# Performance work log

Hardware: AMD Instinct MI355X
Metric: run time of the kernel (lower is better)

## Reference

```python
import jax, jax.numpy as jnp
import numpy as np

B, S, N, D = 4, 30, 2000, 32
HD = 64        # hidden_dim
HEADS = 4
E = 128000


def setup_inputs() -> dict:
    key = jax.random.key(0)
    ks = iter(jax.random.split(key, 48))
    p = lambda shape: jax.random.normal(next(ks), shape, dtype=jnp.float32) * 0.05
    inp = {}
    inp["x_seq"] = jax.random.normal(next(ks), (B, S, N, D), dtype=jnp.float32)
    inp["edge_index"] = jax.random.randint(next(ks), (2, E), 0, N)
    # Bidirectional 2-layer LSTM params (torch gate order i,f,g,o; b = b_ih+b_hh)
    for l, din in [(0, D), (1, 2 * HD)]:
        for d in ("f", "b"):
            inp[f"W_ih_{l}{d}"] = p((4 * HD, din))
            inp[f"W_hh_{l}{d}"] = p((4 * HD, HD))
            inp[f"bias_{l}{d}"] = p((4 * HD,))
    # GAT layer 0: in 2*HD, layer 1: in HD; heads=4, head dim HD, head-averaged output
    inp["gW0"] = p((2 * HD, HEADS * HD))
    inp["ga_src0"] = p((HEADS, HD)); inp["ga_dst0"] = p((HEADS, HD)); inp["gb0"] = p((HD,))
    inp["gW1"] = p((HD, HEADS * HD))
    inp["ga_src1"] = p((HEADS, HD)); inp["ga_dst1"] = p((HEADS, HD)); inp["gb1"] = p((HD,))
    # fc_out: Linear(HD, HD//2) -> ReLU -> Linear(HD//2, 1)
    inp["fW1"] = p((HD // 2, HD)); inp["fb1"] = p((HD // 2,))
    inp["fW2"] = p((1, HD // 2)); inp["fb2"] = p((1,))
    return inp


def _lstm_dir(x, W_ih, W_hh, b, reverse):
    # x: [BN, S, Din] -> hidden states [BN, S, H]
    pre = jnp.einsum('bsd,gd->sbg', x, W_ih) + b  # input projection, [S, BN, 4H]
    BN = x.shape[0]
    H = W_hh.shape[1]

    def step(carry, xt):
        h, c = carry
        g = xt + h @ W_hh.T
        i, f, gg, o = jnp.split(g, 4, axis=-1)
        c = jax.nn.sigmoid(f) * c + jax.nn.sigmoid(i) * jnp.tanh(gg)
        h = jax.nn.sigmoid(o) * jnp.tanh(c)
        return (h, c), h

    init = (jnp.zeros((BN, H), x.dtype), jnp.zeros((BN, H), x.dtype))
    _, hs = jax.lax.scan(step, init, pre, reverse=reverse)
    return jnp.transpose(hs, (1, 0, 2))  # [BN, S, H]


def _gat(x, W, a_src, a_dst, bias, src, dst, num_nodes):
    # edge-wise gather -> attention -> scatter-softmax -> scatter-sum; head-averaged
    Hh, C = a_src.shape
    xp = (x @ W).reshape(-1, Hh, C)                       # [Nn, H, C]
    e = jax.nn.leaky_relu(
        jnp.einsum('nhc,hc->nh', xp, a_src)[src]
        + jnp.einsum('nhc,hc->nh', xp, a_dst)[dst], 0.2)  # [E, H]
    emax = jax.ops.segment_max(e, dst, num_segments=num_nodes)
    w = jnp.exp(e - emax[dst])
    denom = jax.ops.segment_sum(w, dst, num_segments=num_nodes)
    out = jax.ops.segment_sum(w[:, :, None] * xp[src], dst, num_segments=num_nodes)
    out = out / (denom[:, :, None] + 1e-16)
    return out.mean(axis=1) + bias                        # [Nn, C]


def reference(x_seq, edge_index,
              W_ih_0f, W_hh_0f, bias_0f, W_ih_0b, W_hh_0b, bias_0b,
              W_ih_1f, W_hh_1f, bias_1f, W_ih_1b, W_hh_1b, bias_1b,
              gW0, ga_src0, ga_dst0, gb0, gW1, ga_src1, ga_dst1, gb1,
              fW1, fb1, fW2, fb2):
    B_, S_, N_, D_ = x_seq.shape
    x = jnp.transpose(x_seq, (0, 2, 1, 3)).reshape(B_ * N_, S_, D_)
    # bidirectional 2-layer LSTM (eval mode, dropout off)
    h0 = jnp.concatenate([_lstm_dir(x, W_ih_0f, W_hh_0f, bias_0f, False),
                          _lstm_dir(x, W_ih_0b, W_hh_0b, bias_0b, True)], axis=-1)
    h1 = jnp.concatenate([_lstm_dir(h0, W_ih_1f, W_hh_1f, bias_1f, False),
                          _lstm_dir(h0, W_ih_1b, W_hh_1b, bias_1b, True)], axis=-1)
    last = h1[:, -1, :]                                   # [B*N, 2*HD]
    # batch edge_index with per-graph node offsets + self loops (PyG default)
    offs = (jnp.arange(B_) * N_)[None, :, None]
    ei = (edge_index[:, None, :] + offs).reshape(2, -1)
    loops = jnp.arange(B_ * N_)
    src = jnp.concatenate([ei[0], loops])
    dst = jnp.concatenate([ei[1], loops])
    x = jax.nn.relu(_gat(last, gW0, ga_src0, ga_dst0, gb0, src, dst, B_ * N_))
    x = jax.nn.relu(_gat(x, gW1, ga_src1, ga_dst1, gb1, src, dst, B_ * N_))
    x = x.reshape(B_, N_, -1).mean(axis=1)                # mean-pool over nodes
    h = jax.nn.relu(x @ fW1.T + fb1)
    return h @ fW2.T + fb2                                # [B, 1]
```

## Files before the change

kernel.cpp:

```cpp
#include <hip/hip_runtime.h>
#include <cstdint>

#define NN 2000
#define BB 4
#define SEQ 30
#define NODES (BB*NN)
#define EPB 128000
#define NEDGE (BB*EPB + NODES)

constexpr size_t WP0 = 96 * 256;
constexpr size_t WP1 = 192 * 256;
constexpr size_t OFF_WP0F = 0;
constexpr size_t OFF_WP0B = OFF_WP0F + WP0;
constexpr size_t OFF_WP1F = OFF_WP0B + WP0;
constexpr size_t OFF_WP1B = OFF_WP1F + WP1;
constexpr size_t OFF_BP0F = OFF_WP1B + WP1;
constexpr size_t OFF_BP0B = OFF_BP0F + 256;
constexpr size_t OFF_BP1F = OFF_BP0B + 256;
constexpr size_t OFF_BP1B = OFF_BP1F + 256;
constexpr size_t OFF_H0   = OFF_BP1B + 256;
constexpr size_t OFF_LAST = OFF_H0 + (size_t)NODES * SEQ * 128;
constexpr size_t OFF_XP   = OFF_LAST + (size_t)NODES * 128;
constexpr size_t OFF_AS   = OFF_XP + (size_t)NODES * 256;
constexpr size_t OFF_AD   = OFF_AS + (size_t)NODES * 4;
constexpr size_t OFF_F1   = OFF_AD + (size_t)NODES * 4;
constexpr size_t OFF_F2   = OFF_F1 + (size_t)NODES * 64;
constexpr size_t OFF_INT  = OFF_F2 + (size_t)NODES * 64;
constexpr size_t IOFF_CNT  = 0;
constexpr size_t IOFF_OFFS = 8192;
constexpr size_t IOFF_CUR  = 16384;
constexpr size_t IOFF_SSRC = 24576;

__device__ __forceinline__ float rdlane(float v, int k) {
  return __uint_as_float((unsigned)__builtin_amdgcn_readlane((int)__float_as_uint(v), k));
}
__device__ __forceinline__ float sigf(float x) { return 1.f / (1.f + __expf(-x)); }
__device__ __forceinline__ float tanhfast(float x) { return 1.f - 2.f / (__expf(2.f * x) + 1.f); }
__device__ __forceinline__ void fma4(float4& a, float s, const float4& w) {
  a.x = fmaf(s, w.x, a.x); a.y = fmaf(s, w.y, a.y);
  a.z = fmaf(s, w.z, a.z); a.w = fmaf(s, w.w, a.w);
}

__global__ void permute_w(const float* __restrict__ Wih, const float* __restrict__ Whh,
                          const float* __restrict__ bias, float* __restrict__ wp,
                          float* __restrict__ bp, int DIN) {
  const int k = blockIdx.x;
  const int c = threadIdx.x;
  const int jj = c >> 2, q = c & 3;
  const int g = q * 64 + jj;
  const float v = (k < DIN) ? Wih[g * DIN + k] : Whh[g * 64 + (k - DIN)];
  wp[k * 256 + c] = v;
  if (k == 0) bp[c] = bias[g];
}

template<int DIN, bool WRITE_ALL>
__global__ __launch_bounds__(256)
void lstm_scan(const float* __restrict__ xin,
               const float* __restrict__ wpF, const float* __restrict__ wpB,
               const float* __restrict__ bpF, const float* __restrict__ bpB,
               float* __restrict__ hout) {
  constexpr int M = 8;
  __shared__ float whh[64 * 256];
  const int dir = blockIdx.y;
  const float* __restrict__ wp = dir ? wpB : wpF;
  const float* __restrict__ bp = dir ? bpB : bpF;
  {
    const float4* src = (const float4*)(wp + DIN * 256);
    float4* dst = (float4*)whh;
    for (int idx = threadIdx.x; idx < 64 * 256 / 4; idx += 256) dst[idx] = src[idx];
  }
  __syncthreads();

  const int wv = threadIdx.x >> 6;
  const int j  = threadIdx.x & 63;
  const int n0 = (blockIdx.x * 4 + wv) * M;
  const int dirOff = dir * 64;
  const float4 bias4 = *(const float4*)(bp + 4 * j);

  float hreg[M], creg[M];
#pragma unroll
  for (int m = 0; m < M; ++m) { hreg[m] = 0.f; creg[m] = 0.f; }

  int xbase[M];
#pragma unroll
  for (int m = 0; m < M; ++m) {
    const int n = n0 + m;
    if (DIN == 32) {
      const int b = n / NN, node = n - b * NN;
      xbase[m] = (b * SEQ * NN + node) * 32 + (j & 31);
    } else {
      xbase[m] = n * SEQ * 128 + j;
    }
  }

  int steps = SEQ;
  const bool rev = (dir != 0);
  if (!WRITE_ALL && dir) steps = 1;

  for (int t = 0; t < steps; ++t) {
    const int s = rev ? (SEQ - 1 - t) : t;

    float xr0[M], xr1[M];
#pragma unroll
    for (int m = 0; m < M; ++m) {
      if (DIN == 32) {
        xr0[m] = xin[xbase[m] + s * (NN * 32)];
        xr1[m] = 0.f;
      } else {
        xr0[m] = xin[xbase[m] + s * 128];
        xr1[m] = xin[xbase[m] + s * 128 + 64];
      }
    }

    float4 acc[M];
#pragma unroll
    for (int m = 0; m < M; ++m) acc[m] = bias4;

    if (DIN == 32) {
#pragma unroll 8
      for (int k = 0; k < 32; ++k) {
        const float4 w4 = *(const float4*)(wp + k * 256 + 4 * j);
#pragma unroll
        for (int m = 0; m < M; ++m) fma4(acc[m], rdlane(xr0[m], k), w4);
      }
    } else {
#pragma unroll 8
      for (int k = 0; k < 64; ++k) {
        const float4 w4 = *(const float4*)(wp + k * 256 + 4 * j);
#pragma unroll
        for (int m = 0; m < M; ++m) fma4(acc[m], rdlane(xr0[m], k), w4);
      }
#pragma unroll 8
      for (int k = 0; k < 64; ++k) {
        const float4 w4 = *(const float4*)(wp + (64 + k) * 256 + 4 * j);
#pragma unroll
        for (int m = 0; m < M; ++m) fma4(acc[m], rdlane(xr1[m], k), w4);
      }
    }

#pragma unroll 8
    for (int k = 0; k < 64; ++k) {
      const float4 w4 = *(const float4*)(whh + k * 256 + 4 * j);
#pragma unroll
      for (int m = 0; m < M; ++m) fma4(acc[m], rdlane(hreg[m], k), w4);
    }

#pragma unroll
    for (int m = 0; m < M; ++m) {
      const float iv = sigf(acc[m].x);
      const float fv = sigf(acc[m].y);
      const float gv = tanhfast(acc[m].z);
      const float ov = sigf(acc[m].w);
      const float c = fv * creg[m] + iv * gv;
      const float h = ov * tanhfast(c);
      creg[m] = c; hreg[m] = h;
      if (WRITE_ALL) hout[((size_t)(n0 + m) * SEQ + s) * 128 + dirOff + j] = h;
    }
  }
  if (!WRITE_ALL) {
#pragma unroll
    for (int m = 0; m < M; ++m) hout[(size_t)(n0 + m) * 128 + dirOff + j] = hreg[m];
  }
}

__global__ void csr_zero(int* cnt) {
  const int i = blockIdx.x * 256 + threadIdx.x;
  if (i < NODES + 1) cnt[i] = 0;
}
__global__ void csr_count(const int* __restrict__ ei, int* __restrict__ cnt) {
  const int e = blockIdx.x * 256 + threadIdx.x;
  if (e >= NEDGE) return;
  int dst;
  if (e < BB * EPB) { const int b = e / EPB, i = e - b * EPB; dst = ei[EPB + i] + b * NN; }
  else dst = e - BB * EPB;
  atomicAdd(&cnt[dst], 1);
}
__global__ void csr_scan(const int* __restrict__ cnt, int* __restrict__ offs, int* __restrict__ cur) {
  __shared__ int sums[1024];
  const int t = threadIdx.x;
  const int base = t * 8;
  int loc[8]; int s = 0;
#pragma unroll
  for (int i = 0; i < 8; ++i) {
    const int v = (base + i < NODES) ? cnt[base + i] : 0;
    loc[i] = s; s += v;
  }
  sums[t] = s; __syncthreads();
  for (int off = 1; off < 1024; off <<= 1) {
    int v = 0;
    if (t >= off) v = sums[t - off];
    __syncthreads();
    sums[t] += v;
    __syncthreads();
  }
  const int pre = (t == 0) ? 0 : sums[t - 1];
#pragma unroll
  for (int i = 0; i < 8; ++i) {
    if (base + i < NODES) { const int o = pre + loc[i]; offs[base + i] = o; cur[base + i] = o; }
  }
  if (t == 1023) offs[NODES] = sums[1023];
}
__global__ void csr_fill(const int* __restrict__ ei, int* __restrict__ cur, int* __restrict__ ssrc) {
  const int e = blockIdx.x * 256 + threadIdx.x;
  if (e >= NEDGE) return;
  int src, dst;
  if (e < BB * EPB) {
    const int b = e / EPB, i = e - b * EPB;
    src = ei[i] + b * NN; dst = ei[EPB + i] + b * NN;
  } else { src = dst = e - BB * EPB; }
  const int pos = atomicAdd(&cur[dst], 1);
  ssrc[pos] = src;
}

template<int F>
__global__ __launch_bounds__(256)
void gat_prep(const float* __restrict__ feat, const float* __restrict__ gW,
              const float* __restrict__ asrc, const float* __restrict__ adst,
              float* __restrict__ xp, float* __restrict__ as_, float* __restrict__ ad_) {
  __shared__ float xrow[8 * F];
  const int n0 = blockIdx.x * 8;
  for (int idx = threadIdx.x; idx < 8 * F; idx += 256) xrow[idx] = feat[(size_t)n0 * F + idx];
  __syncthreads();
  const int g = threadIdx.x;
  float acc[8];
#pragma unroll
  for (int m = 0; m < 8; ++m) acc[m] = 0.f;
  for (int d = 0; d < F; ++d) {
    const float w = gW[d * 256 + g];
#pragma unroll
    for (int m = 0; m < 8; ++m) acc[m] = fmaf(xrow[m * F + d], w, acc[m]);
  }
#pragma unroll
  for (int m = 0; m < 8; ++m) xp[(size_t)(n0 + m) * 256 + g] = acc[m];
  const float av = asrc[g], dv = adst[g];
  const int h = g >> 6;
#pragma unroll
  for (int m = 0; m < 8; ++m) {
    float s1 = acc[m] * av, s2 = acc[m] * dv;
#pragma unroll
    for (int off = 1; off < 64; off <<= 1) {
      s1 += __shfl_xor(s1, off);
      s2 += __shfl_xor(s2, off);
    }
    if ((g & 63) == 0) {
      as_[(n0 + m) * 4 + h] = s1;
      ad_[(n0 + m) * 4 + h] = s2;
    }
  }
}

__global__ __launch_bounds__(256)
void gat_agg(const int* __restrict__ offs, const int* __restrict__ ssrc,
             const float* __restrict__ as_, const float* __restrict__ ad_,
             const float* __restrict__ xp, const float* __restrict__ gbias,
             float* __restrict__ outf) {
  const int v = blockIdx.x * 4 + (threadIdx.x >> 6);
  const int lane = threadIdx.x & 63;
  const int beg = offs[v], end = offs[v + 1];
  const float4 adv = *(const float4*)(ad_ + v * 4);

  float m0 = -1e30f, m1 = -1e30f, m2 = -1e30f, m3 = -1e30f;
  for (int i = beg + lane; i < end; i += 64) {
    const int sn = ssrc[i];
    const float4 asv = *(const float4*)(as_ + sn * 4);
    float e;
    e = asv.x + adv.x; e = e > 0.f ? e : 0.2f * e; m0 = fmaxf(m0, e);
    e = asv.y + adv.y; e = e > 0.f ? e : 0.2f * e; m1 = fmaxf(m1, e);
    e = asv.z + adv.z; e = e > 0.f ? e : 0.2f * e; m2 = fmaxf(m2, e);
    e = asv.w + adv.w; e = e > 0.f ? e : 0.2f * e; m3 = fmaxf(m3, e);
  }
#pragma unroll
  for (int off = 1; off < 64; off <<= 1) {
    m0 = fmaxf(m0, __shfl_xor(m0, off));
    m1 = fmaxf(m1, __shfl_xor(m1, off));
    m2 = fmaxf(m2, __shfl_xor(m2, off));
    m3 = fmaxf(m3, __shfl_xor(m3, off));
  }

  float a0 = 0, a1 = 0, a2 = 0, a3 = 0, d0 = 0, d1 = 0, d2 = 0, d3 = 0;
  for (int i = beg; i < end; ++i) {
    const int sn = ssrc[i];
    const float4 asv = *(const float4*)(as_ + sn * 4);
    const float* xr = xp + (size_t)sn * 256;
    float e, w;
    e = asv.x + adv.x; e = e > 0.f ? e : 0.2f * e; w = __expf(e - m0); d0 += w; a0 = fmaf(w, xr[lane], a0);
    e = asv.y + adv.y; e = e > 0.f ? e : 0.2f * e; w = __expf(e - m1); d1 += w; a1 = fmaf(w, xr[64 + lane], a1);
    e = asv.z + adv.z; e = e > 0.f ? e : 0.2f * e; w = __expf(e - m2); d2 += w; a2 = fmaf(w, xr[128 + lane], a2);
    e = asv.w + adv.w; e = e > 0.f ? e : 0.2f * e; w = __expf(e - m3); d3 += w; a3 = fmaf(w, xr[192 + lane], a3);
  }
  const float r = 0.25f * (a0 / (d0 + 1e-16f) + a1 / (d1 + 1e-16f) +
                           a2 / (d2 + 1e-16f) + a3 / (d3 + 1e-16f)) + gbias[lane];
  outf[(size_t)v * 64 + lane] = fmaxf(r, 0.f);
}

__global__ void final_mlp(const float* __restrict__ feat2,
                          const float* __restrict__ fW1, const float* __restrict__ fb1,
                          const float* __restrict__ fW2, const float* __restrict__ fb2,
                          float* __restrict__ out) {
  const int b = blockIdx.x;
  __shared__ float part[4][64];
  __shared__ float y[64];
  __shared__ float hh[32];
  const int t = threadIdx.x;
  const int c = t & 63, r = t >> 6;
  float s = 0.f;
  for (int i = r; i < NN; i += 4) s += feat2[(size_t)(b * NN + i) * 64 + c];
  part[r][c] = s; __syncthreads();
  if (t < 64) y[t] = (part[0][t] + part[1][t] + part[2][t] + part[3][t]) * (1.0f / NN);
  __syncthreads();
  if (t < 32) {
    float a = fb1[t];
    for (int cc = 0; cc < 64; ++cc) a = fmaf(y[cc], fW1[t * 64 + cc], a);
    hh[t] = fmaxf(a, 0.f);
  }
  __syncthreads();
  if (t == 0) {
    float o = fb2[0];
    for (int jj = 0; jj < 32; ++jj) o = fmaf(hh[jj], fW2[jj], o);
    out[b] = o;
  }
}

extern "C" void kernel_launch(void* const* d_in, const int* in_sizes, int n_in,
                              void* d_out, int out_size, void* d_ws, size_t ws_size,
                              hipStream_t stream) {
  const float* x_seq = (const float*)d_in[0];
  const int*   ei    = (const int*)d_in[1];
  const float* Wih0f = (const float*)d_in[2];  const float* Whh0f = (const float*)d_in[3];  const float* b0f = (const float*)d_in[4];
  const float* Wih0b = (const float*)d_in[5];  const float* Whh0b = (const float*)d_in[6];  const float* b0b = (const float*)d_in[7];
  const float* Wih1f = (const float*)d_in[8];  const float* Whh1f = (const float*)d_in[9];  const float* b1f = (const float*)d_in[10];
  const float* Wih1b = (const float*)d_in[11]; const float* Whh1b = (const float*)d_in[12]; const float* b1b = (const float*)d_in[13];
  const float* gW0 = (const float*)d_in[14]; const float* gas0 = (const float*)d_in[15];
  const float* gad0 = (const float*)d_in[16]; const float* gb0 = (const float*)d_in[17];
  const float* gW1 = (const float*)d_in[18]; const float* gas1 = (const float*)d_in[19];
  const float* gad1 = (const float*)d_in[20]; const float* gb1 = (const float*)d_in[21];
  const float* fW1 = (const float*)d_in[22]; const float* fb1 = (const float*)d_in[23];
  const float* fW2 = (const float*)d_in[24]; const float* fb2 = (const float*)d_in[25];

  float* ws = (float*)d_ws;
  float* wp0f = ws + OFF_WP0F; float* wp0b = ws + OFF_WP0B;
  float* wp1f = ws + OFF_WP1F; float* wp1b = ws + OFF_WP1B;
  float* bp0f = ws + OFF_BP0F; float* bp0b = ws + OFF_BP0B;
  float* bp1f = ws + OFF_BP1F; float* bp1b = ws + OFF_BP1B;
  float* h0   = ws + OFF_H0;   float* last = ws + OFF_LAST;
  float* xp   = ws + OFF_XP;   float* as_  = ws + OFF_AS;  float* ad_ = ws + OFF_AD;
  float* f1   = ws + OFF_F1;   float* f2   = ws + OFF_F2;
  int* iws  = (int*)(ws + OFF_INT);
  int* cnt  = iws + IOFF_CNT;  int* offs = iws + IOFF_OFFS;
  int* cur  = iws + IOFF_CUR;  int* ssrc = iws + IOFF_SSRC;

  permute_w<<<96, 256, 0, stream>>>(Wih0f, Whh0f, b0f, wp0f, bp0f, 32);
  permute_w<<<96, 256, 0, stream>>>(Wih0b, Whh0b, b0b, wp0b, bp0b, 32);
  permute_w<<<192, 256, 0, stream>>>(Wih1f, Whh1f, b1f, wp1f, bp1f, 128);
  permute_w<<<192, 256, 0, stream>>>(Wih1b, Whh1b, b1b, wp1b, bp1b, 128);

  lstm_scan<32, true><<<dim3(250, 2), 256, 0, stream>>>(x_seq, wp0f, wp0b, bp0f, bp0b, h0);
  lstm_scan<128, false><<<dim3(250, 2), 256, 0, stream>>>(h0, wp1f, wp1b, bp1f, bp1b, last);

  csr_zero<<<32, 256, 0, stream>>>(cnt);
  csr_count<<<(NEDGE + 255) / 256, 256, 0, stream>>>(ei, cnt);
  csr_scan<<<1, 1024, 0, stream>>>(cnt, offs, cur);
  csr_fill<<<(NEDGE + 255) / 256, 256, 0, stream>>>(ei, cur, ssrc);

  gat_prep<128><<<1000, 256, 0, stream>>>(last, gW0, gas0, gad0, xp, as_, ad_);
  gat_agg<<<2000, 256, 0, stream>>>(offs, ssrc, as_, ad_, xp, gb0, f1);
  gat_prep<64><<<1000, 256, 0, stream>>>(f1, gW1, gas1, gad1, xp, as_, ad_);
  gat_agg<<<2000, 256, 0, stream>>>(offs, ssrc, as_, ad_, xp, gb1, f2);

  final_mlp<<<4, 256, 0, stream>>>(f2, fW1, fb1, fW2, fb2, (float*)d_out);
}
```

Baseline: 1.288 ms.

## Convert LSTM scan to packed fp16 dot2 with LDS-resident weights

Weights, inputs and the hidden state are packed into fp16 pairs, and the LSTM matmuls use v_dot2 (fdot2) with fp32 accumulation, halving the multiply-accumulate count and memory traffic. All input and recurrent weights now sit in LDS, and the next step's input is prefetched. Blocks grow to 512 threads with 4 nodes per wave instead of 8, and the layer-0 hidden sequence is stored as packed fp16. This reduces precision of the LSTM inputs and states, which may affect accuracy.

```diff
diff --git a/kernel.cpp b/kernel.cpp
--- a/kernel.cpp
+++ b/kernel.cpp
@@ -8,141 +8,153 @@
 #define EPB 128000
 #define NEDGE (BB*EPB + NODES)
 
-constexpr size_t WP0 = 96 * 256;
-constexpr size_t WP1 = 192 * 256;
-constexpr size_t OFF_WP0F = 0;
-constexpr size_t OFF_WP0B = OFF_WP0F + WP0;
-constexpr size_t OFF_WP1F = OFF_WP0B + WP0;
-constexpr size_t OFF_WP1B = OFF_WP1F + WP1;
-constexpr size_t OFF_BP0F = OFF_WP1B + WP1;
-constexpr size_t OFF_BP0B = OFF_BP0F + 256;
-constexpr size_t OFF_BP1F = OFF_BP0B + 256;
-constexpr size_t OFF_BP1B = OFF_BP1F + 256;
-constexpr size_t OFF_H0   = OFF_BP1B + 256;
-constexpr size_t OFF_LAST = OFF_H0 + (size_t)NODES * SEQ * 128;
-constexpr size_t OFF_XP   = OFF_LAST + (size_t)NODES * 128;
-constexpr size_t OFF_AS   = OFF_XP + (size_t)NODES * 256;
-constexpr size_t OFF_AD   = OFF_AS + (size_t)NODES * 4;
-constexpr size_t OFF_F1   = OFF_AD + (size_t)NODES * 4;
-constexpr size_t OFF_F2   = OFF_F1 + (size_t)NODES * 64;
-constexpr size_t OFF_INT  = OFF_F2 + (size_t)NODES * 64;
+constexpr size_t U_WPH0F = 0;
+constexpr size_t U_WPH0B = U_WPH0F + 48 * 256;
+constexpr size_t U_WPH1F = U_WPH0B + 48 * 256;
+constexpr size_t U_WPH1B = U_WPH1F + 96 * 256;
+constexpr size_t U_BP0F  = U_WPH1B + 96 * 256;
+constexpr size_t U_BP0B  = U_BP0F + 256;
+constexpr size_t U_BP1F  = U_BP0B + 256;
+constexpr size_t U_BP1B  = U_BP1F + 256;
+constexpr size_t U_XPK   = U_BP1B + 256;
+constexpr size_t U_H0P   = U_XPK + (size_t)NODES * SEQ * 16;
+constexpr size_t U_LAST  = U_H0P + (size_t)NODES * SEQ * 64;
+constexpr size_t U_XP    = U_LAST + (size_t)NODES * 128;
+constexpr size_t U_AS    = U_XP + (size_t)NODES * 256;
+constexpr size_t U_AD    = U_AS + (size_t)NODES * 4;
+constexpr size_t U_F1    = U_AD + (size_t)NODES * 4;
+constexpr size_t U_F2    = U_F1 + (size_t)NODES * 64;
+constexpr size_t U_INT   = U_F2 + (size_t)NODES * 64;
 constexpr size_t IOFF_CNT  = 0;
 constexpr size_t IOFF_OFFS = 8192;
 constexpr size_t IOFF_CUR  = 16384;
 constexpr size_t IOFF_SSRC = 24576;
 
-__device__ __forceinline__ float rdlane(float v, int k) {
-  return __uint_as_float((unsigned)__builtin_amdgcn_readlane((int)__float_as_uint(v), k));
+typedef _Float16 h2_t __attribute__((ext_vector_type(2)));
+
+#if __has_builtin(__builtin_amdgcn_fdot2)
+__device__ __forceinline__ float fdot2u(uint32_t a, uint32_t b, float c) {
+  return __builtin_amdgcn_fdot2(__builtin_bit_cast(h2_t, a), __builtin_bit_cast(h2_t, b), c, false);
+}
+#else
+__device__ __forceinline__ float fdot2u(uint32_t a, uint32_t b, float c) {
+  h2_t x = __builtin_bit_cast(h2_t, a), y = __builtin_bit_cast(h2_t, b);
+  return fmaf((float)x[1], (float)y[1], fmaf((float)x[0], (float)y[0], c));
+}
+#endif
+__device__ __forceinline__ uint32_t pk16(float a, float b) {
+  return __builtin_bit_cast(uint32_t, __builtin_amdgcn_cvt_pkrtz(a, b));
+}
+__device__ __forceinline__ uint32_t rdlu(uint32_t v, int k) {
+  return (uint32_t)__builtin_amdgcn_readlane((int)v, k);
 }
 __device__ __forceinline__ float sigf(float x) { return 1.f / (1.f + __expf(-x)); }
 __device__ __forceinline__ float tanhfast(float x) { return 1.f - 2.f / (__expf(2.f * x) + 1.f); }
-__device__ __forceinline__ void fma4(float4& a, float s, const float4& w) {
-  a.x = fmaf(s, w.x, a.x); a.y = fmaf(s, w.y, a.y);
-  a.z = fmaf(s, w.z, a.z); a.w = fmaf(s, w.w, a.w);
-}
-
-__global__ void permute_w(const float* __restrict__ Wih, const float* __restrict__ Whh,
-                          const float* __restrict__ bias, float* __restrict__ wp,
-                          float* __restrict__ bp, int DIN) {
-  const int k = blockIdx.x;
+
+__global__ void permute_pack(const float* __restrict__ Wih, const float* __restrict__ Whh,
+                             const float* __restrict__ bias, uint32_t* __restrict__ wph,
+                             float* __restrict__ bp, int DIN) {
+  const int kp = blockIdx.x;
   const int c = threadIdx.x;
-  const int jj = c >> 2, q = c & 3;
-  const int g = q * 64 + jj;
-  const float v = (k < DIN) ? Wih[g * DIN + k] : Whh[g * 64 + (k - DIN)];
-  wp[k * 256 + c] = v;
-  if (k == 0) bp[c] = bias[g];
-}
-
-template<int DIN, bool WRITE_ALL>
-__global__ __launch_bounds__(256)
-void lstm_scan(const float* __restrict__ xin,
-               const float* __restrict__ wpF, const float* __restrict__ wpB,
+  const int j = c >> 2, q = c & 3;
+  const int g = q * 64 + j;
+  const int k0 = 2 * kp;
+  float a, b;
+  if (k0 < DIN) { a = Wih[g * DIN + k0]; b = Wih[g * DIN + k0 + 1]; }
+  else { const int r = k0 - DIN; a = Whh[g * 64 + r]; b = Whh[g * 64 + r + 1]; }
+  wph[kp * 256 + c] = pk16(a, b);
+  if (kp == 0) bp[c] = bias[g];
+}
+
+__global__ void pack_x(const float* __restrict__ x, uint32_t* __restrict__ out, int n) {
+  const int i = blockIdx.x * 256 + threadIdx.x;
+  if (i < n) out[i] = pk16(x[2 * i], x[2 * i + 1]);
+}
+
+template<int DIN, bool WRITE_ALL, int M>
+__global__ __launch_bounds__(512)
+void lstm_scan(const uint32_t* __restrict__ xpk,
+               const uint32_t* __restrict__ wpF, const uint32_t* __restrict__ wpB,
                const float* __restrict__ bpF, const float* __restrict__ bpB,
-               float* __restrict__ hout) {
-  constexpr int M = 8;
-  __shared__ float whh[64 * 256];
+               float* __restrict__ lastout, uint32_t* __restrict__ hpkout) {
+  constexpr int KPX = DIN / 2;
+  constexpr int KP  = KPX + 32;
+  __shared__ __align__(16) uint32_t wph[KP * 256];
   const int dir = blockIdx.y;
-  const float* __restrict__ wp = dir ? wpB : wpF;
+  const uint32_t* __restrict__ wp = dir ? wpB : wpF;
   const float* __restrict__ bp = dir ? bpB : bpF;
-  {
-    const float4* src = (const float4*)(wp + DIN * 256);
-    float4* dst = (float4*)whh;
-    for (int idx = threadIdx.x; idx < 64 * 256 / 4; idx += 256) dst[idx] = src[idx];
-  }
+  for (int idx = threadIdx.x; idx < KP * 64; idx += 512)
+    ((uint4*)wph)[idx] = ((const uint4*)wp)[idx];
   __syncthreads();
 
   const int wv = threadIdx.x >> 6;
   const int j  = threadIdx.x & 63;
-  const int n0 = (blockIdx.x * 4 + wv) * M;
-  const int dirOff = dir * 64;
+  const int n0 = (blockIdx.x * 8 + wv) * M;
   const float4 bias4 = *(const float4*)(bp + 4 * j);
 
   float hreg[M], creg[M];
-#pragma unroll
-  for (int m = 0; m < M; ++m) { hreg[m] = 0.f; creg[m] = 0.f; }
-
+  uint32_t hpk[M];
+#pragma unroll
+  for (int m = 0; m < M; ++m) { hreg[m] = 0.f; creg[m] = 0.f; hpk[m] = 0u; }
+
+  constexpr int XS = (DIN == 32) ? NN * 16 : 64;
   int xbase[M];
 #pragma unroll
   for (int m = 0; m < M; ++m) {
     const int n = n0 + m;
     if (DIN == 32) {
       const int b = n / NN, node = n - b * NN;
-      xbase[m] = (b * SEQ * NN + node) * 32 + (j & 31);
+      xbase[m] = (b * SEQ * NN + node) * 16 + (j & 15);
     } else {
-      xbase[m] = n * SEQ * 128 + j;
-    }
-  }
-
-  int steps = SEQ;
+      xbase[m] = (n * SEQ) * 64 + j;
+    }
+  }
+
   const bool rev = (dir != 0);
-  if (!WRITE_ALL && dir) steps = 1;
-
-  for (int t = 0; t < steps; ++t) {
-    const int s = rev ? (SEQ - 1 - t) : t;
-
-    float xr0[M], xr1[M];
-#pragma unroll
-    for (int m = 0; m < M; ++m) {
-      if (DIN == 32) {
-        xr0[m] = xin[xbase[m] + s * (NN * 32)];
-        xr1[m] = 0.f;
-      } else {
-        xr0[m] = xin[xbase[m] + s * 128];
-        xr1[m] = xin[xbase[m] + s * 128 + 64];
+  const int steps = (!WRITE_ALL && rev) ? 1 : SEQ;
+  const int sstep = rev ? -1 : 1;
+  int s = rev ? SEQ - 1 : 0;
+
+  uint32_t xu[M];
+#pragma unroll
+  for (int m = 0; m < M; ++m) xu[m] = xpk[xbase[m] + s * XS];
+
+  for (int t = 0; t < steps; ++t, s += sstep) {
+    uint32_t xun[M];
+#pragma unroll
+    for (int m = 0; m < M; ++m) xun[m] = xu[m];
+    if (t + 1 < steps) {
+#pragma unroll
+      for (int m = 0; m < M; ++m) xun[m] = xpk[xbase[m] + (s + sstep) * XS];
+    }
+
+    float4 acc[M];
+#pragma unroll
+    for (int m = 0; m < M; ++m) acc[m] = bias4;
+
+#pragma unroll 2
+    for (int kp = 0; kp < KPX; ++kp) {
+      const uint4 w4 = *(const uint4*)&wph[kp * 256 + 4 * j];
+#pragma unroll
+      for (int m = 0; m < M; ++m) {
+        const uint32_t b2 = rdlu(xu[m], kp);
+        acc[m].x = fdot2u(w4.x, b2, acc[m].x);
+        acc[m].y = fdot2u(w4.y, b2, acc[m].y);
+        acc[m].z = fdot2u(w4.z, b2, acc[m].z);
+        acc[m].w = fdot2u(w4.w, b2, acc[m].w);
       }
     }
-
-    float4 acc[M];
-#pragma unroll
-    for (int m = 0; m < M; ++m) acc[m] = bias4;
-
-    if (DIN == 32) {
-#pragma unroll 8
-      for (int k = 0; k < 32; ++k) {
-        const float4 w4 = *(const float4*)(wp + k * 256 + 4 * j);
-#pragma unroll
-        for (int m = 0; m < M; ++m) fma4(acc[m], rdlane(xr0[m], k), w4);
+#pragma unroll 2
+    for (int kh = 0; kh < 32; ++kh) {
+      const uint4 w4 = *(const uint4*)&wph[(KPX + kh) * 256 + 4 * j];
+#pragma unroll
+      for (int m = 0; m < M; ++m) {
+        const uint32_t b2 = rdlu(hpk[m], 2 * kh);
+        acc[m].x = fdot2u(w4.x, b2, acc[m].x);
+        acc[m].y = fdot2u(w4.y, b2, acc[m].y);
+        acc[m].z = fdot2u(w4.z, b2, acc[m].z);
+        acc[m].w = fdot2u(w4.w, b2, acc[m].w);
       }
-    } else {
-#pragma unroll 8
-      for (int k = 0; k < 64; ++k) {
-        const float4 w4 = *(const float4*)(wp + k * 256 + 4 * j);
-#pragma unroll
-        for (int m = 0; m < M; ++m) fma4(acc[m], rdlane(xr0[m], k), w4);
-      }
-#pragma unroll 8
-      for (int k = 0; k < 64; ++k) {
-        const float4 w4 = *(const float4*)(wp + (64 + k) * 256 + 4 * j);
-#pragma unroll
-        for (int m = 0; m < M; ++m) fma4(acc[m], rdlane(xr1[m], k), w4);
-      }
-    }
-
-#pragma unroll 8
-    for (int k = 0; k < 64; ++k) {
-      const float4 w4 = *(const float4*)(whh + k * 256 + 4 * j);
-#pragma unroll
-      for (int m = 0; m < M; ++m) fma4(acc[m], rdlane(hreg[m], k), w4);
     }
 
 #pragma unroll
@@ -154,12 +166,18 @@
       const float c = fv * creg[m] + iv * gv;
       const float h = ov * tanhfast(c);
       creg[m] = c; hreg[m] = h;
-      if (WRITE_ALL) hout[((size_t)(n0 + m) * SEQ + s) * 128 + dirOff + j] = h;
-    }
+      const float hn = __shfl_down(h, 1);
+      hpk[m] = pk16(h, hn);
+      if (WRITE_ALL && (j & 1) == 0)
+        hpkout[((size_t)(n0 + m) * SEQ + s) * 64 + dir * 32 + (j >> 1)] = hpk[m];
+    }
+#pragma unroll
+    for (int m = 0; m < M; ++m) xu[m] = xun[m];
   }
   if (!WRITE_ALL) {
 #pragma unroll
-    for (int m = 0; m < M; ++m) hout[(size_t)(n0 + m) * 128 + dirOff + j] = hreg[m];
+    for (int m = 0; m < M; ++m)
+      lastout[(size_t)(n0 + m) * 128 + dir * 64 + j] = hreg[m];
   }
 }
 
@@ -337,25 +355,30 @@
   const float* fW1 = (const float*)d_in[22]; const float* fb1 = (const float*)d_in[23];
   const float* fW2 = (const float*)d_in[24]; const float* fb2 = (const float*)d_in[25];
 
-  float* ws = (float*)d_ws;
-  float* wp0f = ws + OFF_WP0F; float* wp0b = ws + OFF_WP0B;
-  float* wp1f = ws + OFF_WP1F; float* wp1b = ws + OFF_WP1B;
-  float* bp0f = ws + OFF_BP0F; float* bp0b = ws + OFF_BP0B;
-  float* bp1f = ws + OFF_BP1F; float* bp1b = ws + OFF_BP1B;
-  float* h0   = ws + OFF_H0;   float* last = ws + OFF_LAST;
-  float* xp   = ws + OFF_XP;   float* as_  = ws + OFF_AS;  float* ad_ = ws + OFF_AD;
-  float* f1   = ws + OFF_F1;   float* f2   = ws + OFF_F2;
-  int* iws  = (int*)(ws + OFF_INT);
+  uint32_t* wsu = (uint32_t*)d_ws;
+  float*    wsf = (float*)d_ws;
+  uint32_t* wph0f = wsu + U_WPH0F; uint32_t* wph0b = wsu + U_WPH0B;
+  uint32_t* wph1f = wsu + U_WPH1F; uint32_t* wph1b = wsu + U_WPH1B;
+  float* bp0f = wsf + U_BP0F; float* bp0b = wsf + U_BP0B;
+  float* bp1f = wsf + U_BP1F; float* bp1b = wsf + U_BP1B;
+  uint32_t* xpk = wsu + U_XPK;
+  uint32_t* h0p = wsu + U_H0P;
+  float* last = wsf + U_LAST;
+  float* xp   = wsf + U_XP;
+  float* as_  = wsf + U_AS;  float* ad_ = wsf + U_AD;
+  float* f1   = wsf + U_F1;  float* f2  = wsf + U_F2;
+  int* iws  = (int*)(wsf + U_INT);
   int* cnt  = iws + IOFF_CNT;  int* offs = iws + IOFF_OFFS;
   int* cur  = iws + IOFF_CUR;  int* ssrc = iws + IOFF_SSRC;
 
-  permute_w<<<96, 256, 0, stream>>>(Wih0f, Whh0f, b0f, wp0f, bp0f, 32);
-  permute_w<<<96, 256, 0, stream>>>(Wih0b, Whh0b, b0b, wp0b, bp0b, 32);
-  permute_w<<<192, 256, 0, stream>>>(Wih1f, Whh1f, b1f, wp1f, bp1f, 128);
-  permute_w<<<192, 256, 0, stream>>>(Wih1b, Whh1b, b1b, wp1b, bp1b, 128);
-
-  lstm_scan<32, true><<<dim3(250, 2), 256, 0, stream>>>(x_seq, wp0f, wp0b, bp0f, bp0b, h0);
-  lstm_scan<128, false><<<dim3(250, 2), 256, 0, stream>>>(h0, wp1f, wp1b, bp1f, bp1b, last);
+  permute_pack<<<48, 256, 0, stream>>>(Wih0f, Whh0f, b0f, wph0f, bp0f, 32);
+  permute_pack<<<48, 256, 0, stream>>>(Wih0b, Whh0b, b0b, wph0b, bp0b, 32);
+  permute_pack<<<96, 256, 0, stream>>>(Wih1f, Whh1f, b1f, wph1f, bp1f, 128);
+  permute_pack<<<96, 256, 0, stream>>>(Wih1b, Whh1b, b1b, wph1b, bp1b, 128);
+  pack_x<<<(NODES * SEQ * 16 + 255) / 256, 256, 0, stream>>>(x_seq, xpk, NODES * SEQ * 16);
+
+  lstm_scan<32, true, 4><<<dim3(250, 2), 512, 0, stream>>>(xpk, wph0f, wph0b, bp0f, bp0b, nullptr, h0p);
+  lstm_scan<128, false, 4><<<dim3(250, 2), 512, 0, stream>>>(h0p, wph1f, wph1b, bp1f, bp1b, last, nullptr);
 
   csr_zero<<<32, 256, 0, stream>>>(cnt);
   csr_count<<<(NEDGE + 255) / 256, 256, 0, stream>>>(ei, cnt);
```

Measured after the change: 1.102 ms. -14.4%, faster.
